# Performance work log

Hardware: AMD Instinct MI355X
Metric: run time of the kernel (lower is better)

Reference implementation:

```python
import jax, jax.numpy as jnp
import numpy as np

EPS = 1e-6
T = 10.0
STEPS = 3
BN_EPS = 1e-5

def _normalize(x, axis):
    n = jnp.sqrt(jnp.sum(x * x, axis=axis, keepdims=True))
    return x / jnp.maximum(n, EPS)

def _vq_step(X, D):
    # X: (B, d, n), D: (B, d, r)
    Dn = _normalize(D, 1)
    Xn = _normalize(X, 1)
    cos = jnp.einsum('bdr,bdn->brn', Dn, Xn)          # (B, r, n)
    C = jax.nn.softmax(cos / T, axis=1)               # softmax over r
    XCt = jnp.einsum('bdn,brn->bdr', X, C)            # (B, d, r)
    sums = jnp.maximum(jnp.sum(C, axis=2), EPS)       # (B, r)
    D2 = _normalize(XCt / sums[:, None, :], 1)
    Xbar = jnp.einsum('bdr,brn->bdn', D2, C)
    return D2, C, Xbar

def _ham_vq(X, D0):
    # K-1 steps without gradient tracking, final step with grad through X only
    Xs = jax.lax.stop_gradient(X)
    def body(D, _):
        D, _, _ = _vq_step(Xs, D)
        return D, None
    D, _ = jax.lax.scan(body, _normalize(D0, 1), None, length=STEPS - 1)
    D = jax.lax.stop_gradient(D)
    _, _, Xbar = _vq_step(X, D)
    return Xbar

def _conv1x1(x, w, b=None):
    y = jnp.einsum('oc,bchw->bohw', w, x)
    if b is not None:
        y = y + b[None, :, None, None]
    return y

def _bn(x, gamma, beta, mean, var):
    inv = gamma / jnp.sqrt(var + BN_EPS)
    return x * inv[None, :, None, None] + (beta - mean * inv)[None, :, None, None]


def setup_inputs() -> dict:
    key = jax.random.key(0)
    ks = jax.random.split(key, 16)
    B, Cin, H, W = 8, 512, 64, 64
    d_mid, r = 512, 64
    out_ch = 2 * d_mid  # dual
    sc = 0.02
    inp = {
        'z': jax.random.normal(ks[0], (B, Cin, H, W), jnp.float32),
        'lower_w': jax.random.normal(ks[1], (out_ch, Cin), jnp.float32) * sc,
        'lower_b': jnp.zeros((out_ch,), jnp.float32),
        'Dinit_s': jax.random.uniform(ks[2], (B, d_mid, r), jnp.float32),
        'Dinit_c': jax.random.uniform(ks[3], (B, d_mid, r), jnp.float32),
        'cheese_w': jax.random.normal(ks[4], (out_ch, out_ch), jnp.float32) * sc,
        'ch_gamma': jnp.ones((out_ch,), jnp.float32),
        'ch_beta': jnp.zeros((out_ch,), jnp.float32),
        'ch_mean': jax.random.normal(ks[5], (out_ch,), jnp.float32) * 0.1,
        'ch_var': jax.random.uniform(ks[6], (out_ch,), jnp.float32) + 0.5,
        'upper_w': jax.random.normal(ks[7], (Cin, out_ch), jnp.float32) * sc,
        'upper_b': jnp.zeros((Cin,), jnp.float32),
        'h_gamma': jnp.ones((Cin,), jnp.float32),
        'h_beta': jnp.zeros((Cin,), jnp.float32),
        'h_mean': jax.random.normal(ks[8], (Cin,), jnp.float32) * 0.1,
        'h_var': jax.random.uniform(ks[9], (Cin,), jnp.float32) + 0.5,
        'coef_ham': jnp.array(1.0, jnp.float32),
        'coef_shortcut': jnp.array(1.0, jnp.float32),
    }
    return inp


def reference(z, lower_w, lower_b, Dinit_s, Dinit_c, cheese_w,
              ch_gamma, ch_beta, ch_mean, ch_var, upper_w, upper_b,
              h_gamma, h_beta, h_mean, h_var, coef_ham, coef_shortcut):
    B, Cin, H, W = z.shape
    identity = z
    # lower: conv1x1 + relu
    y = jax.nn.relu(_conv1x1(z, lower_w, lower_b))       # (B, 2*d_mid, H, W)
    d_mid = y.shape[1] // 2
    y1, y2 = y[:, :d_mid], y[:, d_mid:]
    n = H * W
    # spatial ham
    Xs = y1.reshape(B, d_mid, n)
    y1 = _ham_vq(Xs, Dinit_s).reshape(B, d_mid, H, W)
    # channel ham (same (B, d, n) flattening; HamMD requires dim1 == d_mid)
    Xc = y2.reshape(B, d_mid, n)
    y2 = _ham_vq(Xc, Dinit_c).reshape(B, d_mid, H, W)
    y = jnp.concatenate([y1, y2], axis=1)
    # cheese: conv1x1(no bias) + BN + relu
    y = jax.nn.relu(_bn(_conv1x1(y, cheese_w), ch_gamma, ch_beta, ch_mean, ch_var))
    # upper conv1x1 + BN
    h = _bn(_conv1x1(y, upper_w, upper_b), h_gamma, h_beta, h_mean, h_var)
    out = coef_ham * h + coef_shortcut * identity
    return jax.nn.relu(out)
```

## Files before the change

### kernel.cpp

```cpp
#include <hip/hip_runtime.h>
#include <hip/hip_bf16.h>

typedef __bf16 bf16_t;
typedef __bf16 bf16x4 __attribute__((ext_vector_type(4)));
typedef __bf16 bf16x8 __attribute__((ext_vector_type(8)));
typedef float  f32x4  __attribute__((ext_vector_type(4)));

#define HEPS 1e-6f

__device__ __forceinline__ void gload16(const bf16_t* g, bf16_t* l) {
    __builtin_amdgcn_global_load_lds(
        (const __attribute__((address_space(1))) unsigned int*)(g),
        (__attribute__((address_space(3))) unsigned int*)(l),
        16, 0, 0);
}


__global__ void cvt_all_k(const float* __restrict__ wl, bf16_t* __restrict__ dwl,
                          const float* __restrict__ wc, bf16_t* __restrict__ dwc,
                          const float* __restrict__ wu, bf16_t* __restrict__ dwu) {
    int i = blockIdx.x * 256 + threadIdx.x;
    if (i < 524288) dwl[i] = (bf16_t)wl[i];
    else if (i < 1572864) { int k = i - 524288; dwc[k] = (bf16_t)wc[k]; }
    else { int k = i - 1572864; dwu[k] = (bf16_t)wu[k]; }
}

__global__ void prep_k(const float* __restrict__ chg, const float* __restrict__ chb,
                       const float* __restrict__ chm, const float* __restrict__ chv,
                       const float* __restrict__ hg, const float* __restrict__ hb,
                       const float* __restrict__ hm, const float* __restrict__ hv,
                       const float* __restrict__ ub, const float* __restrict__ cham,
                       float* __restrict__ chA, float* __restrict__ chB,
                       float* __restrict__ hA2, float* __restrict__ hB2) {
    int i = blockIdx.x * 256 + threadIdx.x;
    if (i < 1024) {
        float inv = chg[i] * rsqrtf(chv[i] + 1e-5f);
        chA[i] = inv;
        chB[i] = chb[i] - chm[i] * inv;
    }
    if (i < 512) {
        float inv = hg[i] * rsqrtf(hv[i] + 1e-5f);
        float cA = cham[0];
        hA2[i] = cA * inv;
        hB2[i] = cA * (fmaf(ub[i], inv, hb[i]) - hm[i] * inv);
    }
}

__global__ void tz_k(const float* __restrict__ z, bf16_t* __restrict__ Zt,
                     bf16_t* __restrict__ zb) {
    __shared__ bf16_t t[64][68];
    int b = blockIdx.z, kt = blockIdx.y, nt = blockIdx.x;
    const size_t boff = ((size_t)b * 512 + kt * 64) * 4096 + nt * 64;
    const float* src = z + boff;
    bf16_t* zbo = zb + boff;
    int tid = threadIdx.x;
    int kr = tid >> 4;
    int nc = (tid & 15) * 4;
    #pragma unroll
    for (int it = 0; it < 4; ++it) {
        int k = kr + it * 16;
        float4 v = *(const float4*)&src[(size_t)k * 4096 + nc];
        bf16x4 o;
        o[0] = (bf16_t)v.x; o[1] = (bf16_t)v.y; o[2] = (bf16_t)v.z; o[3] = (bf16_t)v.w;
        t[nc + 0][k] = o[0]; t[nc + 1][k] = o[1];
        t[nc + 2][k] = o[2]; t[nc + 3][k] = o[3];
        *(bf16x4*)&zbo[(size_t)k * 4096 + nc] = o;
    }
    __syncthreads();
    bf16_t* dst = Zt + ((size_t)b * 4096 + nt * 64) * 512 + kt * 64;
    int nr = tid >> 4;
    int kc = (tid & 15) * 4;
    #pragma unroll
    for (int it = 0; it < 4; ++it) {
        int n = nr + it * 16;
        bf16x4 o;
        #pragma unroll
        for (int c = 0; c < 4; ++c) o[c] = t[n][kc + c];
        *(bf16x4*)&dst[(size_t)n * 512 + kc] = o;
    }
}

__global__ void dinit_k(const float* __restrict__ Ds, const float* __restrict__ Dc,
                        bf16_t* __restrict__ Dt) {
    int bs = blockIdx.y;
    int b = bs >> 1;
    const float* src = ((bs & 1) ? Dc : Ds) + (size_t)b * 512 * 64;
    int idx = blockIdx.x * 256 + threadIdx.x;
    int r = idx & 63, d = idx >> 6;
    Dt[(size_t)bs * 64 * 512 + (size_t)r * 512 + d] = (bf16_t)src[d * 64 + r];
}

__global__ void dnorm_k(const bf16_t* __restrict__ Dt, float* __restrict__ dinv) {
    int gw = (blockIdx.x * 256 + threadIdx.x) >> 6;
    int lane = threadIdx.x & 63;
    bf16x8 v = *(const bf16x8*)(Dt + (size_t)gw * 512 + lane * 8);
    float s = 0.f;
    #pragma unroll
    for (int e = 0; e < 8; ++e) { float f = (float)v[e]; s += f * f; }
    #pragma unroll
    for (int off = 32; off > 0; off >>= 1) s += __shfl_xor(s, off);
    if (lane == 0) dinv[gw] = 1.0f / fmaxf(sqrtf(s), HEPS);
}

__global__ void reduce_k(const float* __restrict__ P, bf16_t* __restrict__ Dt,
                         float* __restrict__ dinv) {
    int bsr = blockIdx.x;
    int bs = bsr >> 6, r = bsr & 63;
    int lane = threadIdx.x;
    const float* base = P + ((size_t)(bs * 8) * 64 + r) * 512 + lane * 8;
    float s[8] = {0.f, 0.f, 0.f, 0.f, 0.f, 0.f, 0.f, 0.f};
    #pragma unroll
    for (int kc = 0; kc < 8; ++kc) {
        const float* p = base + (size_t)kc * 64 * 512;
        float4 u = *(const float4*)p;
        float4 w = *(const float4*)(p + 4);
        s[0] += u.x; s[1] += u.y; s[2] += u.z; s[3] += u.w;
        s[4] += w.x; s[5] += w.y; s[6] += w.z; s[7] += w.w;
    }
    bf16x8 o;
    float sq = 0.f;
    #pragma unroll
    for (int e = 0; e < 8; ++e) { sq += s[e] * s[e]; o[e] = (bf16_t)s[e]; }
    *(bf16x8*)&Dt[(size_t)bsr * 512 + lane * 8] = o;
    #pragma unroll
    for (int off = 32; off > 0; off >>= 1) sq += __shfl_xor(sq, off);
    if (lane == 0) dinv[bsr] = 1.0f / fmaxf(sqrtf(sq), HEPS);
}

template<int BM, int BN, int WAVES_M, int WAVES_N, int EPI, int ORDER>
__launch_bounds__(256)
__global__ void g2(const bf16_t* __restrict__ Ag, const bf16_t* __restrict__ Bg,
                   void* __restrict__ Cg, void* __restrict__ C2g,
                   const int M, const int N, const int K,
                   const int ldA, const int ldB, const int ldC,
                   const long aStride, const long bStride,
                   const long cStride, const long c2Stride,
                   const float* __restrict__ p0, const float* __restrict__ p1,
                   const float* __restrict__ scal,
                   const void* __restrict__ shortcut, const long sStride)
{
    constexpr int WM = BM / WAVES_M, WN = BN / WAVES_N;
    constexpr int FM = WM / 16, FN = WN / 16;
    constexpr int ASEG = BM / 64, BSEG = BN / 64;
    constexpr int LPT = ASEG + BSEG;

    __shared__ __align__(64) bf16_t SH[3 * (BM + BN) * 32];
    __shared__ float dl[64];
    bf16_t* Al = SH;
    bf16_t* Bl = SH + 3 * BM * 32;

    const int tid = threadIdx.x;
    const int wave = tid >> 6, lane = tid & 63;
    const int l15 = lane & 15, q = lane >> 4;
    const int lrow = lane >> 2, lcol = (lane & 3) * 8;

    const int gx = gridDim.x, gy = gridDim.y;
    const int per = gx * gy;
    const int nwg = per * gridDim.z;
    const int g = blockIdx.z * per + blockIdx.y * gx + blockIdx.x;
    const int qq = nwg >> 3, rr = nwg & 7;
    const int xcd = g & 7, jj = g >> 3;
    const int w = (xcd < rr ? xcd * (qq + 1) : rr * (qq + 1) + (xcd - rr) * qq) + jj;
    const int bz = w / per;
    const int rem = w - bz * per;
    int bx, by;
    if constexpr (ORDER == 0) { by = rem / gx; bx = rem - by * gx; }
    else                      { bx = rem / gy; by = rem - bx * gy; }

    int bs = bz, exA = 0, exB = 0;
    if constexpr (EPI == 5) { bs = bz >> 3; exA = exB = (bz & 7) * 512; }
    if constexpr (EPI == 7) { exA = (bz & 1) * 512; }

    const int n0 = bx * BN;
    const int m0 = by * BM;
    const int wm0 = (wave / WAVES_N) * WM;
    const int wn0 = (wave % WAVES_N) * WN;

    const bf16_t* Ab;
    const bf16_t* Bb;
    if constexpr (EPI == 6) {
        Ab = Ag + (size_t)(bz >> 1) * (size_t)aStride + (size_t)(bz & 1) * 512;
        Bb = Bg + (size_t)bz * (size_t)bStride;
    } else {
        Ab = Ag + (size_t)bs * (size_t)aStride + exA;
        Bb = Bg + (size_t)bs * (size_t)bStride + exB;
    }

    if constexpr (EPI == 6) { if (tid < 64) dl[tid] = p0[bz * 64 + tid]; }

    auto stage = [&](int buf, int k0) {
        #pragma unroll
        for (int t = 0; t < ASEG; ++t) {
            int seg = wave * ASEG + t;
            gload16(Ab + (size_t)(m0 + seg * 16 + lrow) * ldA + k0 + lcol,
                    &Al[buf * BM * 32 + seg * 512]);
        }
        #pragma unroll
        for (int t = 0; t < BSEG; ++t) {
            int seg = wave * BSEG + t;
            gload16(Bb + (size_t)(n0 + seg * 16 + lrow) * ldB + k0 + lcol,
                    &Bl[buf * BN * 32 + seg * 512]);
        }
    };

    f32x4 acc[FM][FN];
    #pragma unroll
    for (int i = 0; i < FM; ++i)
        #pragma unroll
        for (int j = 0; j < FN; ++j)
            #pragma unroll
            for (int e = 0; e < 4; ++e) acc[i][j][e] = 0.f;

    float xsq[FM];
    #pragma unroll
    for (int i = 0; i < FM; ++i) xsq[i] = 0.f;

    const int nK = K / 32;
    stage(0, 0);
    if (nK > 1) stage(1, 32);

    for (int t = 0; t < nK; ++t) {
        const int cur = t % 3;

        if (t < nK - 1) asm volatile("s_waitcnt vmcnt(%0)" :: "i"(LPT) : "memory");
        else            asm volatile("s_waitcnt vmcnt(0)" ::: "memory");
        asm volatile("s_barrier" ::: "memory");
        __builtin_amdgcn_sched_barrier(0);

        if (t + 2 < nK) stage((t + 2) % 3, (t + 2) * 32);

        bf16x8 af[FM], bfm[FN];
        #pragma unroll
        for (int i = 0; i < FM; ++i)
            af[i] = *(const bf16x8*)&Al[cur * BM * 32 + (wm0 + 16 * i + l15) * 32 + 8 * q];
        #pragma unroll
        for (int j = 0; j < FN; ++j)
            bfm[j] = *(const bf16x8*)&Bl[cur * BN * 32 + (wn0 + 16 * j + l15) * 32 + 8 * q];

        if constexpr (EPI == 6) {
            #pragma unroll
            for (int i = 0; i < FM; ++i)
                #pragma unroll
                for (int e = 0; e < 8; ++e) {
                    float f = (float)af[i][e];
                    xsq[i] = fmaf(f, f, xsq[i]);
                }
        }

        __builtin_amdgcn_s_setprio(1);
        #pragma unroll
        for (int i = 0; i < FM; ++i)
            #pragma unroll
            for (int j = 0; j < FN; ++j)
                acc[i][j] = __builtin_amdgcn_mfma_f32_16x16x32_bf16(af[i], bfm[j], acc[i][j], 0, 0, 0);
        __builtin_amdgcn_s_setprio(0);
    }

    int rowB[FM];
    #pragma unroll
    for (int i = 0; i < FM; ++i) rowB[i] = m0 + wm0 + 16 * i + 4 * q;
    const int colBase = n0 + wn0;

    if constexpr (EPI == 2) {
        bf16_t* O = (bf16_t*)Cg + (size_t)bz * (size_t)cStride;
        #pragma unroll
        for (int j = 0; j < FN; ++j) {
            int col = colBase + 16 * j + l15;
            float a = p0[col], b = p1[col];
            #pragma unroll
            for (int i = 0; i < FM; ++i) {
                int rb = rowB[i];
                #pragma unroll
                for (int e = 0; e < 4; ++e) {
                    float v = fmaxf(fmaf(acc[i][j][e], a, b), 0.f);
                    O[(size_t)(rb + e) * ldC + col] = (bf16_t)v;
                }
            }
        }
    } else if constexpr (EPI == 3) {
        float* O = (float*)Cg + (size_t)bz * (size_t)cStride;
        const bf16_t* scg = (const bf16_t*)shortcut + (size_t)bz * (size_t)sStride;
        bf16_t* SP = SH;
        float cB = scal[0];
        __syncthreads();
        {
            int row = tid >> 1, h = tid & 1;
            #pragma unroll
            for (int u = 0; u < 8; ++u)
                *(bf16x8*)&SP[row * 132 + h * 64 + u * 8] =
                    *(const bf16x8*)&scg[(size_t)(m0 + row) * ldC + n0 + h * 64 + u * 8];
        }
        __syncthreads();
        #pragma unroll
        for (int i = 0; i < FM; ++i) {
            int rl = wm0 + 16 * i + 4 * q;
            #pragma unroll
            for (int e = 0; e < 4; ++e) {
                int row = m0 + rl + e;
                float a = p0[row], b = p1[row];
                #pragma unroll
                for (int j = 0; j < FN; ++j) {
                    int cl = wn0 + 16 * j + l15;
                    float v = fmaf(acc[i][j][e], a, b)
                            + cB * (float)SP[(rl + e) * 132 + cl];
                    O[(size_t)row * ldC + n0 + cl] = fmaxf(v, 0.f);
                }
            }
        }
    } else if constexpr (EPI == 5) {
        float* O = (float*)Cg + (size_t)bz * (size_t)cStride;
        #pragma unroll
        for (int i = 0; i < FM; ++i) {
            int rb = rowB[i];
            #pragma unroll
            for (int j = 0; j < FN; ++j) {
                int col = colBase + 16 * j + l15;
                *(f32x4*)&O[(size_t)col * ldC + rb] = acc[i][j];
            }
        }
    } else if constexpr (EPI == 6) {
        bf16_t* Cc = (bf16_t*)Cg  + (size_t)bz * (size_t)cStride;
        bf16_t* Ct = (bf16_t*)C2g + (size_t)(bz >> 1) * (size_t)c2Stride;
        const int hoff = (bz & 1) * 64;
        const bool doCt = (C2g != nullptr);
        float xs[FM];
        #pragma unroll
        for (int i = 0; i < FM; ++i) {
            float s2 = xsq[i];
            s2 += __shfl_xor(s2, 16);
            s2 += __shfl_xor(s2, 32);
            xs[i] = s2;
        }
        float di[FN];
        #pragma unroll
        for (int j = 0; j < FN; ++j) di[j] = dl[16 * j + l15];
        #pragma unroll
        for (int i = 0; i < FM; ++i) {
            int rb = rowB[i];
            bf16x4 tj[FN];
            #pragma unroll
            for (int e = 0; e < 4; ++e) {
                float s2row = __shfl(xs[i], 4 * q + e);
                float xi = 1.0f / (10.0f * fmaxf(sqrtf(s2row), HEPS));
                float v[FN];
                float mx = -1e30f;
                #pragma unroll
                for (int j = 0; j < FN; ++j) {
                    v[j] = acc[i][j][e] * di[j] * xi;
                    mx = fmaxf(mx, v[j]);
                }
                mx = fmaxf(mx, __shfl_xor(mx, 1));
                mx = fmaxf(mx, __shfl_xor(mx, 2));
                mx = fmaxf(mx, __shfl_xor(mx, 4));
                mx = fmaxf(mx, __shfl_xor(mx, 8));
                float sm = 0.f;
                #pragma unroll
                for (int j = 0; j < FN; ++j) { v[j] = __expf(v[j] - mx); sm += v[j]; }
                sm += __shfl_xor(sm, 1);
                sm += __shfl_xor(sm, 2);
                sm += __shfl_xor(sm, 4);
                sm += __shfl_xor(sm, 8);
                float rs = 1.0f / sm;
                #pragma unroll
                for (int j = 0; j < FN; ++j) {
                    float p = v[j] * rs;
                    tj[j][e] = (bf16_t)p;
                    if (doCt) Ct[(size_t)(rb + e) * 128 + hoff + 16 * j + l15] = (bf16_t)p;
                }
            }
            #pragma unroll
            for (int j = 0; j < FN; ++j)
                *(bf16x4*)&Cc[(size_t)(16 * j + l15) * ldC + rb] = tj[j];
        }
    } else if constexpr (EPI == 7) {
        bf16_t* O = (bf16_t*)Cg + (size_t)(bz >> 1) * (size_t)cStride;
        const int hoff = (bz & 1) * 64;
        #pragma unroll
        for (int j = 0; j < FN; ++j) {
            int col = colBase + 16 * j + l15;
            float di = p0[bz * 64 + col];
            #pragma unroll
            for (int i = 0; i < FM; ++i) {
                int rb = rowB[i];
                #pragma unroll
                for (int e = 0; e < 4; ++e)
                    O[(size_t)(rb + e) * 128 + hoff + col] = (bf16_t)(acc[i][j][e] * di);
            }
        }
    } else if constexpr (EPI == 8) {
        bf16_t* O  = (bf16_t*)Cg  + (size_t)bz * (size_t)cStride;
        bf16_t* O2 = (bf16_t*)C2g + (size_t)bz * (size_t)c2Stride;
        #pragma unroll
        for (int j = 0; j < FN; ++j) {
            int col = colBase + 16 * j + l15;
            float bias = p0[col];
            #pragma unroll
            for (int i = 0; i < FM; ++i) {
                int rb = rowB[i];
                bf16x4 t;
                #pragma unroll
                for (int e = 0; e < 4; ++e) {
                    float v = fmaxf(acc[i][j][e] + bias, 0.f);
                    t[e] = (bf16_t)v;
                    O[(size_t)(rb + e) * ldC + col] = t[e];
                }
                *(bf16x4*)&O2[(size_t)col * 4096 + rb] = t;
            }
        }
    }
}


extern "C" void kernel_launch(void* const* d_in, const int* in_sizes, int n_in,
                              void* d_out, int out_size, void* d_ws, size_t ws_size,
                              hipStream_t stream) {
    const float* z        = (const float*)d_in[0];
    const float* lower_w  = (const float*)d_in[1];
    const float* lower_b  = (const float*)d_in[2];
    const float* Dinit_s  = (const float*)d_in[3];
    const float* Dinit_c  = (const float*)d_in[4];
    const float* cheese_w = (const float*)d_in[5];
    const float* ch_gamma = (const float*)d_in[6];
    const float* ch_beta  = (const float*)d_in[7];
    const float* ch_mean  = (const float*)d_in[8];
    const float* ch_var   = (const float*)d_in[9];
    const float* upper_w  = (const float*)d_in[10];
    const float* upper_b  = (const float*)d_in[11];
    const float* h_gamma  = (const float*)d_in[12];
    const float* h_beta   = (const float*)d_in[13];
    const float* h_mean   = (const float*)d_in[14];
    const float* h_var    = (const float*)d_in[15];
    const float* coef_ham = (const float*)d_in[16];
    const float* coef_sc  = (const float*)d_in[17];

    char* ws = (char*)d_ws;
    size_t off = 0;
    auto alloc = [&](size_t bytes) -> void* {
        void* p = ws + off;
        off += (bytes + 255) & ~(size_t)255;
        return p;
    };

    bf16_t* Wl   = (bf16_t*)alloc((size_t)1024 * 512 * 2);
    bf16_t* Wc   = (bf16_t*)alloc((size_t)1024 * 1024 * 2);
    bf16_t* Wu   = (bf16_t*)alloc((size_t)512 * 1024 * 2);
    float*  chA  = (float*) alloc(1024 * 4);
    float*  chB  = (float*) alloc(1024 * 4);
    float*  hA2  = (float*) alloc(512 * 4);
    float*  hB2  = (float*) alloc(512 * 4);
    float*  dinv = (float*) alloc(1024 * 4);
    bf16_t* Xbf  = (bf16_t*)alloc((size_t)8 * 1024 * 4096 * 2);
    bf16_t* Xt   = (bf16_t*)alloc((size_t)8 * 4096 * 1024 * 2);
    bf16_t* Zt   = (bf16_t*)alloc((size_t)8 * 4096 * 512 * 2);
    bf16_t* zb   = (bf16_t*)alloc((size_t)8 * 512 * 4096 * 2);
    bf16_t* Cb   = (bf16_t*)alloc((size_t)16 * 64 * 4096 * 2);
    bf16_t* Ct2  = (bf16_t*)alloc((size_t)8 * 4096 * 128 * 2);
    float*  P    = (float*) alloc((size_t)128 * 64 * 512 * 4);
    bf16_t* Dta  = (bf16_t*)alloc((size_t)16 * 64 * 512 * 2);
    bf16_t* Dtb  = (bf16_t*)alloc((size_t)16 * 64 * 512 * 2);
    bf16_t* Eb   = (bf16_t*)alloc((size_t)8 * 1024 * 128 * 2);
    bf16_t* Ycht = Xbf;

    dim3 blk(256);

    cvt_all_k<<<8192, blk, 0, stream>>>(lower_w, Wl, cheese_w, Wc, upper_w, Wu);
    prep_k<<<4, blk, 0, stream>>>(ch_gamma, ch_beta, ch_mean, ch_var,
                                  h_gamma, h_beta, h_mean, h_var,
                                  upper_b, coef_ham, chA, chB, hA2, hB2);
    tz_k<<<dim3(64, 8, 8), blk, 0, stream>>>(z, Zt, zb);
    dinit_k<<<dim3(128, 16), blk, 0, stream>>>(Dinit_s, Dinit_c, Dta);

    g2<128, 128, 2, 2, 8, 0><<<dim3(8, 32, 8), blk, 0, stream>>>(
        Zt, Wl, (void*)Xt, (void*)Xbf, 4096, 1024, 512,
        512, 512, 1024,
        (long)4096 * 512, 0L, (long)4096 * 1024, (long)1024 * 4096,
        lower_b, nullptr, nullptr, nullptr, 0L);

    dnorm_k<<<256, blk, 0, stream>>>(Dta, dinv);

    bf16_t* cur = Dta;
    bf16_t* nxt = Dtb;
    for (int t = 0; t < 3; ++t) {
        g2<128, 64, 4, 1, 6, 0><<<dim3(1, 32, 16), blk, 0, stream>>>(
            Xt, cur, (void*)Cb, (t == 2) ? (void*)Ct2 : nullptr, 4096, 64, 512,
            1024, 512, 4096,
            (long)4096 * 1024, (long)64 * 512, (long)64 * 4096, (long)4096 * 128,
            dinv, nullptr, nullptr, nullptr, 0L);
        g2<64, 64, 2, 2, 5, 0><<<dim3(1, 8, 128), blk, 0, stream>>>(
            Xbf, Cb, (void*)P, nullptr, 512, 64, 512,
            4096, 4096, 512,
            (long)512 * 4096, (long)64 * 4096, (long)64 * 512, 0L,
            nullptr, nullptr, nullptr, nullptr, 0L);
        reduce_k<<<1024, dim3(64), 0, stream>>>(P, nxt, dinv);
        bf16_t* tmp = cur; cur = nxt; nxt = tmp;
    }

    g2<128, 64, 2, 2, 7, 0><<<dim3(1, 8, 16), blk, 0, stream>>>(
        Wc, cur, (void*)Eb, nullptr, 1024, 64, 512,
        1024, 512, 128,
        0L, (long)64 * 512, (long)1024 * 128, 0L,
        dinv, nullptr, nullptr, nullptr, 0L);

    g2<128, 128, 2, 2, 2, 0><<<dim3(8, 32, 8), blk, 0, stream>>>(
        Ct2, Eb, (void*)Ycht, nullptr, 4096, 1024, 128,
        128, 128, 1024,
        (long)4096 * 128, (long)1024 * 128, (long)4096 * 1024, 0L,
        chA, chB, nullptr, nullptr, 0L);

    g2<128, 128, 2, 2, 3, 1><<<dim3(32, 4, 8), blk, 0, stream>>>(
        Wu, Ycht, d_out, nullptr, 512, 4096, 1024,
        1024, 1024, 4096,
        0L, (long)4096 * 1024, (long)512 * 4096, 0L,
        hA2, hB2, coef_sc, zb, (long)512 * 4096);

    (void)in_sizes; (void)n_in; (void)out_size; (void)ws_size;
}
```

Before: 312.7 us.

## Merge setup kernels and shrink big GEMM tiles to 128x64

Folds weight conversion, dictionary init transpose and BN parameter prep into one launch, removing two kernel launches. The three large GEMMs (lower conv, cheese conv, upper conv) switch from 128x128 to 128x64 tiles with twice as many blocks, and the EPI 3 shortcut staging is generalised to the new tile width. Smaller tiles raise block count and occupancy on a 256-CU part but lower per-block data reuse and add more global reads of the shared operand.

After: 328.5 us. 1.05x slower.

```diff
diff --git a/kernel.cpp b/kernel.cpp
--- a/kernel.cpp
+++ b/kernel.cpp
@@ -15,34 +15,46 @@
         16, 0, 0);
 }
 
-
-__global__ void cvt_all_k(const float* __restrict__ wl, bf16_t* __restrict__ dwl,
-                          const float* __restrict__ wc, bf16_t* __restrict__ dwc,
-                          const float* __restrict__ wu, bf16_t* __restrict__ dwu) {
-    int i = blockIdx.x * 256 + threadIdx.x;
-    if (i < 524288) dwl[i] = (bf16_t)wl[i];
-    else if (i < 1572864) { int k = i - 524288; dwc[k] = (bf16_t)wc[k]; }
-    else { int k = i - 1572864; dwu[k] = (bf16_t)wu[k]; }
-}
-
-__global__ void prep_k(const float* __restrict__ chg, const float* __restrict__ chb,
-                       const float* __restrict__ chm, const float* __restrict__ chv,
-                       const float* __restrict__ hg, const float* __restrict__ hb,
-                       const float* __restrict__ hm, const float* __restrict__ hv,
-                       const float* __restrict__ ub, const float* __restrict__ cham,
-                       float* __restrict__ chA, float* __restrict__ chB,
-                       float* __restrict__ hA2, float* __restrict__ hB2) {
-    int i = blockIdx.x * 256 + threadIdx.x;
-    if (i < 1024) {
-        float inv = chg[i] * rsqrtf(chv[i] + 1e-5f);
-        chA[i] = inv;
-        chB[i] = chb[i] - chm[i] * inv;
-    }
-    if (i < 512) {
-        float inv = hg[i] * rsqrtf(hv[i] + 1e-5f);
-        float cA = cham[0];
-        hA2[i] = cA * inv;
-        hB2[i] = cA * (fmaf(ub[i], inv, hb[i]) - hm[i] * inv);
+__global__ void setup_k(const float* __restrict__ wl, bf16_t* __restrict__ dwl,
+                        const float* __restrict__ wc, bf16_t* __restrict__ dwc,
+                        const float* __restrict__ wu, bf16_t* __restrict__ dwu,
+                        const float* __restrict__ Ds, const float* __restrict__ Dc,
+                        bf16_t* __restrict__ Dt,
+                        const float* __restrict__ chg, const float* __restrict__ chb,
+                        const float* __restrict__ chm, const float* __restrict__ chv,
+                        const float* __restrict__ hg, const float* __restrict__ hb,
+                        const float* __restrict__ hm, const float* __restrict__ hv,
+                        const float* __restrict__ ub, const float* __restrict__ cham,
+                        float* __restrict__ chA, float* __restrict__ chB,
+                        float* __restrict__ hA2, float* __restrict__ hB2) {
+    int bid = blockIdx.x;
+    int tid = threadIdx.x;
+    if (bid < 8192) {
+        int i = bid * 256 + tid;
+        if (i < 524288) dwl[i] = (bf16_t)wl[i];
+        else if (i < 1572864) { int k = i - 524288; dwc[k] = (bf16_t)wc[k]; }
+        else { int k = i - 1572864; dwu[k] = (bf16_t)wu[k]; }
+    } else if (bid < 10240) {
+        int b2 = bid - 8192;
+        int bs = b2 >> 7;
+        int idx = (b2 & 127) * 256 + tid;
+        int b = bs >> 1;
+        const float* src = ((bs & 1) ? Dc : Ds) + (size_t)b * 512 * 64;
+        int r = idx & 63, d = idx >> 6;
+        Dt[(size_t)bs * 64 * 512 + (size_t)r * 512 + d] = (bf16_t)src[d * 64 + r];
+    } else {
+        int i = (bid - 10240) * 256 + tid;
+        if (i < 1024) {
+            float inv = chg[i] * rsqrtf(chv[i] + 1e-5f);
+            chA[i] = inv;
+            chB[i] = chb[i] - chm[i] * inv;
+        }
+        if (i < 512) {
+            float inv = hg[i] * rsqrtf(hv[i] + 1e-5f);
+            float cA = cham[0];
+            hA2[i] = cA * inv;
+            hB2[i] = cA * (fmaf(ub[i], inv, hb[i]) - hm[i] * inv);
+        }
     }
 }
 
@@ -78,16 +90,6 @@
         for (int c = 0; c < 4; ++c) o[c] = t[n][kc + c];
         *(bf16x4*)&dst[(size_t)n * 512 + kc] = o;
     }
-}
-
-__global__ void dinit_k(const float* __restrict__ Ds, const float* __restrict__ Dc,
-                        bf16_t* __restrict__ Dt) {
-    int bs = blockIdx.y;
-    int b = bs >> 1;
-    const float* src = ((bs & 1) ? Dc : Ds) + (size_t)b * 512 * 64;
-    int idx = blockIdx.x * 256 + threadIdx.x;
-    int r = idx & 63, d = idx >> 6;
-    Dt[(size_t)bs * 64 * 512 + (size_t)r * 512 + d] = (bf16_t)src[d * 64 + r];
 }
 
 __global__ void dnorm_k(const bf16_t* __restrict__ Dt, float* __restrict__ dinv) {
@@ -278,17 +280,19 @@
             }
         }
     } else if constexpr (EPI == 3) {
+        constexpr int SPAD = BN + 4;
+        constexpr int V = (BM * BN) / 2048;
         float* O = (float*)Cg + (size_t)bz * (size_t)cStride;
         const bf16_t* scg = (const bf16_t*)shortcut + (size_t)bz * (size_t)sStride;
         bf16_t* SP = SH;
         float cB = scal[0];
         __syncthreads();
-        {
-            int row = tid >> 1, h = tid & 1;
-            #pragma unroll
-            for (int u = 0; u < 8; ++u)
-                *(bf16x8*)&SP[row * 132 + h * 64 + u * 8] =
-                    *(const bf16x8*)&scg[(size_t)(m0 + row) * ldC + n0 + h * 64 + u * 8];
+        #pragma unroll
+        for (int v = 0; v < V; ++v) {
+            int flat = (tid * V + v) * 8;
+            int row = flat / BN, col = flat % BN;
+            *(bf16x8*)&SP[row * SPAD + col] =
+                *(const bf16x8*)&scg[(size_t)(m0 + row) * ldC + n0 + col];
         }
         __syncthreads();
         #pragma unroll
@@ -302,7 +306,7 @@
                 for (int j = 0; j < FN; ++j) {
                     int cl = wn0 + 16 * j + l15;
                     float v = fmaf(acc[i][j][e], a, b)
-                            + cB * (float)SP[(rl + e) * 132 + cl];
+                            + cB * (float)SP[(rl + e) * SPAD + cl];
                     O[(size_t)row * ldC + n0 + cl] = fmaxf(v, 0.f);
                 }
             }
@@ -463,14 +467,14 @@
 
     dim3 blk(256);
 
-    cvt_all_k<<<8192, blk, 0, stream>>>(lower_w, Wl, cheese_w, Wc, upper_w, Wu);
-    prep_k<<<4, blk, 0, stream>>>(ch_gamma, ch_beta, ch_mean, ch_var,
-                                  h_gamma, h_beta, h_mean, h_var,
-                                  upper_b, coef_ham, chA, chB, hA2, hB2);
+    setup_k<<<10244, blk, 0, stream>>>(lower_w, Wl, cheese_w, Wc, upper_w, Wu,
+                                       Dinit_s, Dinit_c, Dta,
+                                       ch_gamma, ch_beta, ch_mean, ch_var,
+                                       h_gamma, h_beta, h_mean, h_var,
+                                       upper_b, coef_ham, chA, chB, hA2, hB2);
     tz_k<<<dim3(64, 8, 8), blk, 0, stream>>>(z, Zt, zb);
-    dinit_k<<<dim3(128, 16), blk, 0, stream>>>(Dinit_s, Dinit_c, Dta);
-
-    g2<128, 128, 2, 2, 8, 0><<<dim3(8, 32, 8), blk, 0, stream>>>(
+
+    g2<128, 64, 2, 2, 8, 0><<<dim3(16, 32, 8), blk, 0, stream>>>(
         Zt, Wl, (void*)Xt, (void*)Xbf, 4096, 1024, 512,
         512, 512, 1024,
         (long)4096 * 512, 0L, (long)4096 * 1024, (long)1024 * 4096,
@@ -501,13 +505,13 @@
         0L, (long)64 * 512, (long)1024 * 128, 0L,
         dinv, nullptr, nullptr, nullptr, 0L);
 
-    g2<128, 128, 2, 2, 2, 0><<<dim3(8, 32, 8), blk, 0, stream>>>(
+    g2<128, 64, 2, 2, 2, 0><<<dim3(16, 32, 8), blk, 0, stream>>>(
         Ct2, Eb, (void*)Ycht, nullptr, 4096, 1024, 128,
         128, 128, 1024,
         (long)4096 * 128, (long)1024 * 128, (long)4096 * 1024, 0L,
         chA, chB, nullptr, nullptr, 0L);
 
-    g2<128, 128, 2, 2, 3, 1><<<dim3(32, 4, 8), blk, 0, stream>>>(
+    g2<128, 64, 2, 2, 3, 1><<<dim3(64, 4, 8), blk, 0, stream>>>(
         Wu, Ycht, d_out, nullptr, 512, 4096, 1024,
         1024, 1024, 4096,
         0L, (long)4096 * 1024, (long)512 * 4096, 0L,
```
